# Performance work log

Hardware: AMD Instinct MI355X
Metric: run time of the kernel (lower is better)

## Reference

```python
import jax, jax.numpy as jnp
import numpy as np

M_PER_GROUP = 16
EPS = 0.001


def setup_inputs() -> dict:
    key = jax.random.key(0)
    x = jax.random.normal(key, (32, 64, 64, 256), dtype=jnp.float32)
    return {"x": x}


def reference(x) -> jnp.ndarray:
    # x: [B, W, H, C] (NHWC). Training-phase path, decomposition='cholesky', renorm=False.
    b, w, h, c = x.shape
    groups = c // M_PER_GROUP
    n = b * w * h  # samples per channel

    # [C, B*W*H]
    x_flat = jnp.transpose(x, (3, 0, 1, 2)).reshape(c, -1)
    mean = jnp.mean(x_flat, axis=1, keepdims=True)          # [C, 1]
    f = x_flat - mean                                        # [C, N]

    # per-group covariance: [G, m, N] -> [G, m, m]
    fg = f.reshape(groups, M_PER_GROUP, -1)
    denom = jnp.float32(n) - 1.0
    cov = jnp.einsum('gmn,gkn->gmk', fg, fg) / denom
    eye = jnp.eye(M_PER_GROUP, dtype=x.dtype)
    cov = (1.0 - EPS) * cov + EPS * eye
    # NOTE: the original TF code divides by (N-1) a second time after shrinkage;
    # reproduced faithfully here.
    cov = cov / denom

    # batched Cholesky + triangular solve: inv_sqrt = L^{-1}
    chol = jnp.linalg.cholesky(cov)                          # [G, m, m], lower
    inv_sqrt = jax.vmap(
        lambda L: jax.scipy.linalg.solve_triangular(L, eye, lower=True)
    )(chol)                                                  # [G, m, m]

    # whiten: [G, m, m] @ [G, m, N] -> [G, m, N]
    f_hat = jnp.einsum('gmk,gkn->gmn', inv_sqrt, fg)
    out = f_hat.reshape(c, b, w, h)
    return jnp.transpose(out, (1, 2, 3, 0))
```

## Files before the change

### kernel.cpp

```cpp
#include <hip/hip_runtime.h>


#define NROWS   131072
#define DENOMF  131071.0f
#define EPSV    0.001f

#define OFF_INV    0
#define OFF_BIAS   4096
#define OFF_RED    4352
#define OFF_PART   151808
#define GS2        9216

typedef __attribute__((ext_vector_type(8))) short bf16x8;
typedef __attribute__((ext_vector_type(4))) float f32x4;
typedef __attribute__((ext_vector_type(4))) unsigned int u32x4;

__device__ __forceinline__ unsigned int fbits(float v) {
    return __builtin_bit_cast(unsigned int, v);
}
__device__ __forceinline__ float bfloat(unsigned int u) {
    return __builtin_bit_cast(float, u);
}

__device__ __forceinline__ void gload_lds16(float* lds, const float* g) {
    __builtin_amdgcn_global_load_lds(
        (const __attribute__((address_space(1))) unsigned int*)g,
        (__attribute__((address_space(3))) unsigned int*)lds, 16, 0, 0);
}

struct Row8 { float a, b, c, d, e, f, g, h; };

__device__ __forceinline__ void cvt8(const Row8 r, bf16x8& hv, bf16x8& lv, float& s) {
    s += ((r.a + r.b) + (r.c + r.d)) + ((r.e + r.f) + (r.g + r.h));
    const unsigned int ua = fbits(r.a), ub = fbits(r.b), uc = fbits(r.c), ud = fbits(r.d);
    const unsigned int ue = fbits(r.e), uf = fbits(r.f), ug = fbits(r.g), uh = fbits(r.h);
    u32x4 hp;
    hp.x = (ub & 0xFFFF0000u) | (ua >> 16);
    hp.y = (ud & 0xFFFF0000u) | (uc >> 16);
    hp.z = (uf & 0xFFFF0000u) | (ue >> 16);
    hp.w = (uh & 0xFFFF0000u) | (ug >> 16);
    const float da = r.a - bfloat(ua & 0xFFFF0000u);
    const float db = r.b - bfloat(ub & 0xFFFF0000u);
    const float dc = r.c - bfloat(uc & 0xFFFF0000u);
    const float dd = r.d - bfloat(ud & 0xFFFF0000u);
    const float de = r.e - bfloat(ue & 0xFFFF0000u);
    const float df = r.f - bfloat(uf & 0xFFFF0000u);
    const float dg = r.g - bfloat(ug & 0xFFFF0000u);
    const float dh = r.h - bfloat(uh & 0xFFFF0000u);
    u32x4 lp;
    lp.x = (fbits(db) & 0xFFFF0000u) | (fbits(da) >> 16);
    lp.y = (fbits(dd) & 0xFFFF0000u) | (fbits(dc) >> 16);
    lp.z = (fbits(df) & 0xFFFF0000u) | (fbits(de) >> 16);
    lp.w = (fbits(dh) & 0xFFFF0000u) | (fbits(dg) >> 16);
    hv = __builtin_bit_cast(bf16x8, hp);
    lv = __builtin_bit_cast(bf16x8, lp);
}

__global__ __launch_bounds__(512, 2) void k1_stats(const float* __restrict__ x,
                                                   float* __restrict__ ws, int NB) {
    __shared__ float xt[2][64 * 260];
    const int tid = threadIdx.x;
    const int lane = tid & 63, wv = tid >> 6;
    const int slot = lane >> 4;
    const int TPB = (NROWS / 64) / NB;
    const size_t tile0 = (size_t)blockIdx.x * TPB;

    const int g0 = wv * 2;
    const int rb0 = g0 * 16 + (lane & 15);
    const int roA0 = (slot * 8 + ((0 + 2 * slot) & 7)) * 260 + rb0;
    const int roA1 = (slot * 8 + ((1 + 2 * slot) & 7)) * 260 + rb0;
    const int roA2 = (slot * 8 + ((2 + 2 * slot) & 7)) * 260 + rb0;
    const int roA3 = (slot * 8 + ((3 + 2 * slot) & 7)) * 260 + rb0;
    const int roA4 = (slot * 8 + ((4 + 2 * slot) & 7)) * 260 + rb0;
    const int roA5 = (slot * 8 + ((5 + 2 * slot) & 7)) * 260 + rb0;
    const int roA6 = (slot * 8 + ((6 + 2 * slot) & 7)) * 260 + rb0;
    const int roA7 = (slot * 8 + ((7 + 2 * slot) & 7)) * 260 + rb0;
    const int roB0 = roA0 + 32 * 260, roB1 = roA1 + 32 * 260;
    const int roB2 = roA2 + 32 * 260, roB3 = roA3 + 32 * 260;
    const int roB4 = roA4 + 32 * 260, roB5 = roA5 + 32 * 260;
    const int roB6 = roA6 + 32 * 260, roB7 = roA7 + 32 * 260;

    f32x4 hh0 = {0,0,0,0}, hl0 = {0,0,0,0}, ll0 = {0,0,0,0};
    f32x4 hh1 = {0,0,0,0}, hl1 = {0,0,0,0}, ll1 = {0,0,0,0};
    float s0 = 0.f, s1 = 0.f;

#define STAGE(B, T)                                                           \
    {                                                                         \
        const float* gp = x + ((tile0 + (T)) * 64 + (size_t)(wv * 8)) * 256   \
                            + (size_t)lane * 4;                               \
        float* lb = &xt[B][(wv * 8) * 260];                                   \
        gload_lds16(lb + 0 * 260, gp + 0 * 256);                              \
        gload_lds16(lb + 1 * 260, gp + 1 * 256);                              \
        gload_lds16(lb + 2 * 260, gp + 2 * 256);                              \
        gload_lds16(lb + 3 * 260, gp + 3 * 256);                              \
        gload_lds16(lb + 4 * 260, gp + 4 * 256);                              \
        gload_lds16(lb + 5 * 260, gp + 5 * 256);                              \
        gload_lds16(lb + 6 * 260, gp + 6 * 256);                              \
        gload_lds16(lb + 7 * 260, gp + 7 * 256);                              \
    }
#define PROCG(BUF, U, G, AHH, AHL, ALL, S)                                    \
    {                                                                         \
        const float* bp = &xt[BUF][0];                                        \
        Row8 r;                                                               \
        r.a = bp[ro##U##0 + (G) * 16]; r.b = bp[ro##U##1 + (G) * 16];         \
        r.c = bp[ro##U##2 + (G) * 16]; r.d = bp[ro##U##3 + (G) * 16];         \
        r.e = bp[ro##U##4 + (G) * 16]; r.f = bp[ro##U##5 + (G) * 16];         \
        r.g = bp[ro##U##6 + (G) * 16]; r.h = bp[ro##U##7 + (G) * 16];         \
        bf16x8 hv, lv;                                                        \
        cvt8(r, hv, lv, S);                                                   \
        AHH = __builtin_amdgcn_mfma_f32_16x16x32_bf16(hv, hv, AHH, 0, 0, 0);  \
        AHL = __builtin_amdgcn_mfma_f32_16x16x32_bf16(hv, lv, AHL, 0, 0, 0);  \
        ALL = __builtin_amdgcn_mfma_f32_16x16x32_bf16(lv, lv, ALL, 0, 0, 0);  \
    }
#define PROC4(BUF)                                                            \
    PROCG(BUF, A, 0, hh0, hl0, ll0, s0);                                      \
    PROCG(BUF, B, 0, hh0, hl0, ll0, s0);                                      \
    PROCG(BUF, A, 1, hh1, hl1, ll1, s1);                                      \
    PROCG(BUF, B, 1, hh1, hl1, ll1, s1);

    STAGE(0, 0);
    for (int t = 0; t < TPB - 1; ++t) {
        __syncthreads();
        STAGE((t + 1) & 1, t + 1);
        PROC4(t & 1);
    }
    __syncthreads();
    PROC4((TPB - 1) & 1);
#undef PROC4
#undef PROCG
#undef STAGE

    float* pb = ws + OFF_PART + (size_t)blockIdx.x * GS2 + (size_t)g0 * 576;
#define STG(G, AHH, AHL, ALL, S)                                              \
    {                                                                         \
        float* pw = pb + (G) * 576;                                           \
        pw[0 * 64 + lane] = AHH[0] + ALL[0];                                  \
        pw[1 * 64 + lane] = AHH[1] + ALL[1];                                  \
        pw[2 * 64 + lane] = AHH[2] + ALL[2];                                  \
        pw[3 * 64 + lane] = AHH[3] + ALL[3];                                  \
        pw[4 * 64 + lane] = AHL[0]; pw[5 * 64 + lane] = AHL[1];               \
        pw[6 * 64 + lane] = AHL[2]; pw[7 * 64 + lane] = AHL[3];               \
        pw[8 * 64 + lane] = S;                                                \
    }
    STG(0, hh0, hl0, ll0, s0);
    STG(1, hh1, hl1, ll1, s1);
#undef STG
}

__global__ __launch_bounds__(256, 4) void k2_reduce(float* __restrict__ ws, int NB) {
    const int t = blockIdx.x * 256 + threadIdx.x;
    if (t >= GS2) return;
    const int per = NB / 16;
    const float* p = ws + OFF_PART + (size_t)(blockIdx.y * per) * GS2 + t;
    float sum = 0.f;
#pragma unroll 8
    for (int b = 0; b < per; ++b) sum += p[(size_t)b * GS2];
    ws[OFF_RED + (size_t)blockIdx.y * GS2 + t] = sum;
}

__device__ __forceinline__ void chol_from_sg(const float* sg, int g, int tid,
                                             float* __restrict__ ws) {
    const int ii = tid & 15;
    const float inv_denom = 1.0f / DENOMF;
    const float cs_ii = sg[512 + ii] + sg[512 + 16 + ii] +
                        sg[512 + 32 + ii] + sg[512 + 48 + ii];
    const float mu_l = cs_ii * (1.0f / (float)NROWS);

#define GIDX2(T, I, J) ((T) * 256 + ((I) & 3) * 64 + ((((I) >> 2)) << 4) + (J))
    float arow[16];
#pragma unroll
    for (int kk = 0; kk < 16; ++kk) {
        float G = sg[GIDX2(0, ii, kk)] + sg[GIDX2(1, ii, kk)] + sg[GIDX2(1, kk, ii)];
        float mu_k = __shfl(mu_l, kk, 64);
        float cv = (G - (float)NROWS * mu_l * mu_k) * inv_denom;
        cv = cv * (1.0f - EPSV) + ((kk == ii) ? EPSV : 0.0f);
        arow[kk] = cv * inv_denom;
    }
#undef GIDX2

    float lrow[16];
#pragma unroll
    for (int j = 0; j < 16; ++j) {
        float diag = __shfl(arow[j], j, 64);
        float ljj  = sqrtf(diag);
        float lij  = (ii == j) ? ljj : arow[j] / ljj;
        lrow[j] = lij;
#pragma unroll
        for (int k = j + 1; k < 16; ++k) {
            float lkj = __shfl(lij, k, 64);
            arow[k] = fmaf(-lij, lkj, arow[k]);
        }
    }

    float xcol[16];
#pragma unroll
    for (int i2 = 0; i2 < 16; ++i2) {
        float ssum = (ii == i2) ? 1.0f : 0.0f;
#pragma unroll
        for (int k = 0; k < 16; ++k) {
            if (k < i2) {
                float Lik = __shfl(lrow[k], i2, 64);
                ssum = fmaf(-Lik, xcol[k], ssum);
            }
        }
        float Lii = __shfl(lrow[i2], i2, 64);
        xcol[i2] = (i2 >= ii) ? ssum / Lii : 0.0f;
    }

    float* invg = ws + OFF_INV + g * 256;
#pragma unroll
    for (int i2 = 0; i2 < 16; ++i2) {
        if (tid < 16) invg[i2 * 16 + tid] = xcol[i2];
        float bi = xcol[i2] * mu_l;
        bi += __shfl_xor(bi, 1, 64);
        bi += __shfl_xor(bi, 2, 64);
        bi += __shfl_xor(bi, 4, 64);
        bi += __shfl_xor(bi, 8, 64);
        if (tid == 0) ws[OFF_BIAS + g * 16 + i2] = bi;
    }
}

__global__ void k2_chol(float* __restrict__ ws, int NB) {
    __shared__ float sg[576];
    const int g = blockIdx.x, tid = threadIdx.x;

    for (int e = tid; e < 576; e += 64) {
        float v = 0.f;
#pragma unroll
        for (int y = 0; y < 16; ++y)
            v += ws[OFF_RED + (size_t)y * GS2 + g * 576 + e];
        sg[e] = v;
    }
    __syncthreads();
    chol_from_sg(sg, g, tid, ws);
}

template <int CTRL>
__device__ __forceinline__ float dpp1(float v) {
    int iv = __builtin_bit_cast(int, v);
    int r = __builtin_amdgcn_update_dpp(iv, iv, CTRL, 0xF, 0xF, false);
    return __builtin_bit_cast(float, r);
}
template <int CTRL>
__device__ __forceinline__ float4 dpp4(float4 v) {
    float4 r;
    r.x = dpp1<CTRL>(v.x);
    r.y = dpp1<CTRL>(v.y);
    r.z = dpp1<CTRL>(v.z);
    r.w = dpp1<CTRL>(v.w);
    return r;
}

#define DOT4(O, A, V) \
    O = fmaf(A.x, V.x, O); O = fmaf(A.y, V.y, O); \
    O = fmaf(A.z, V.z, O); O = fmaf(A.w, V.w, O)

__global__ __launch_bounds__(256, 4) void k3_apply(const float* __restrict__ x,
                                                   const float* __restrict__ ws,
                                                   float* __restrict__ out) {
    const int tid = threadIdx.x, lane = tid & 63, wv = tid >> 6;
    const int q = lane & 3, g = lane >> 2;

    const float* invg = ws + OFF_INV + g * 256;
#define LOADIR(R, M) \
    *reinterpret_cast<const float4*>(invg + (4 * q + (R)) * 16 + 4 * (q ^ (M)))
    float4 ir00 = LOADIR(0, 0), ir01 = LOADIR(0, 1), ir02 = LOADIR(0, 2), ir03 = LOADIR(0, 3);
    float4 ir10 = LOADIR(1, 0), ir11 = LOADIR(1, 1), ir12 = LOADIR(1, 2), ir13 = LOADIR(1, 3);
    float4 ir20 = LOADIR(2, 0), ir21 = LOADIR(2, 1), ir22 = LOADIR(2, 2), ir23 = LOADIR(2, 3);
    float4 ir30 = LOADIR(3, 0), ir31 = LOADIR(3, 1), ir32 = LOADIR(3, 2), ir33 = LOADIR(3, 3);
#undef LOADIR
    float4 b4 = *reinterpret_cast<const float4*>(ws + OFF_BIAS + g * 16 + 4 * q);

    const int rpb   = NROWS / gridDim.x;
    const int iters = rpb / 4;
    const size_t rowbase = (size_t)blockIdx.x * rpb;
    const float4* xp = reinterpret_cast<const float4*>(x) + rowbase * 64 + lane;
    float4*       op = reinterpret_cast<float4*>(out)     + rowbase * 64 + lane;

    float4 cur = xp[(size_t)wv * 64];
    for (int i = 0; i < iters; ++i) {
        const int ip = (i + 1 < iters) ? (i + 1) : (iters - 1);
        float4 nxt = xp[(size_t)(ip * 4 + wv) * 64];

        float4 v0 = cur;
        float4 v1 = dpp4<0xB1>(cur);
        float4 v2 = dpp4<0x4E>(cur);
        float4 v3 = dpp4<0x1B>(cur);

        float o0 = -b4.x, o1 = -b4.y, o2 = -b4.z, o3 = -b4.w;
        DOT4(o0, ir00, v0); DOT4(o0, ir01, v1); DOT4(o0, ir02, v2); DOT4(o0, ir03, v3);
        DOT4(o1, ir10, v0); DOT4(o1, ir11, v1); DOT4(o1, ir12, v2); DOT4(o1, ir13, v3);
        DOT4(o2, ir20, v0); DOT4(o2, ir21, v1); DOT4(o2, ir22, v2); DOT4(o2, ir23, v3);
        DOT4(o3, ir30, v0); DOT4(o3, ir31, v1); DOT4(o3, ir32, v2); DOT4(o3, ir33, v3);

        op[(size_t)(i * 4 + wv) * 64] = make_float4(o0, o1, o2, o3);
        cur = nxt;
    }
}

extern "C" void kernel_launch(void* const* d_in, const int* in_sizes, int n_in,
                              void* d_out, int out_size, void* d_ws, size_t ws_size,
                              hipStream_t stream) {
    const float* x = (const float*)d_in[0];
    float* out = (float*)d_out;
    float* ws  = (float*)d_ws;

    int NB = 128;
    if (ws_size >= (size_t)(OFF_PART + 256 * GS2) * sizeof(float)) NB = 256;

    k1_stats<<<NB, 512, 0, stream>>>(x, ws, NB);
    dim3 rg((GS2 + 255) / 256, 16);
    k2_reduce<<<rg, 256, 0, stream>>>(ws, NB);
    k2_chol<<<16, 64, 0, stream>>>(ws, NB);
    k3_apply<<<1024, 256, 0, stream>>>(x, ws, out);
}
```

Measured before the change: 89.80 us.

## Use 32x32x16 MFMA over group pairs for covariance Gram accumulation

```diff
diff --git a/kernel.cpp b/kernel.cpp
--- a/kernel.cpp
+++ b/kernel.cpp
@@ -8,12 +8,13 @@
 #define OFF_INV    0
 #define OFF_BIAS   4096
 #define OFF_RED    4352
-#define OFF_PART   151808
-#define GS2        9216
-
-typedef __attribute__((ext_vector_type(8))) short bf16x8;
-typedef __attribute__((ext_vector_type(4))) float f32x4;
-typedef __attribute__((ext_vector_type(4))) unsigned int u32x4;
+#define OFF_PART   274688
+#define GS3        16896
+#define PWN3       2112
+
+typedef __attribute__((ext_vector_type(8)))  short bf16x8;
+typedef __attribute__((ext_vector_type(16))) float f32x16;
+typedef __attribute__((ext_vector_type(4)))  unsigned int u32x4;
 
 __device__ __forceinline__ unsigned int fbits(float v) {
     return __builtin_bit_cast(unsigned int, v);
@@ -61,62 +62,46 @@
     __shared__ float xt[2][64 * 260];
     const int tid = threadIdx.x;
     const int lane = tid & 63, wv = tid >> 6;
-    const int slot = lane >> 4;
     const int TPB = (NROWS / 64) / NB;
     const size_t tile0 = (size_t)blockIdx.x * TPB;
 
-    const int g0 = wv * 2;
-    const int rb0 = g0 * 16 + (lane & 15);
-    const int roA0 = (slot * 8 + ((0 + 2 * slot) & 7)) * 260 + rb0;
-    const int roA1 = (slot * 8 + ((1 + 2 * slot) & 7)) * 260 + rb0;
-    const int roA2 = (slot * 8 + ((2 + 2 * slot) & 7)) * 260 + rb0;
-    const int roA3 = (slot * 8 + ((3 + 2 * slot) & 7)) * 260 + rb0;
-    const int roA4 = (slot * 8 + ((4 + 2 * slot) & 7)) * 260 + rb0;
-    const int roA5 = (slot * 8 + ((5 + 2 * slot) & 7)) * 260 + rb0;
-    const int roA6 = (slot * 8 + ((6 + 2 * slot) & 7)) * 260 + rb0;
-    const int roA7 = (slot * 8 + ((7 + 2 * slot) & 7)) * 260 + rb0;
-    const int roB0 = roA0 + 32 * 260, roB1 = roA1 + 32 * 260;
-    const int roB2 = roA2 + 32 * 260, roB3 = roA3 + 32 * 260;
-    const int roB4 = roA4 + 32 * 260, roB5 = roA5 + 32 * 260;
-    const int roB6 = roA6 + 32 * 260, roB7 = roA7 + 32 * 260;
-
-    f32x4 hh0 = {0,0,0,0}, hl0 = {0,0,0,0}, ll0 = {0,0,0,0};
-    f32x4 hh1 = {0,0,0,0}, hl1 = {0,0,0,0}, ll1 = {0,0,0,0};
-    float s0 = 0.f, s1 = 0.f;
+    const int gp = wv;
+    const int hb = (lane >> 5) * 2080 + gp * 32 + (lane & 31);
+
+    f32x16 aHH, aHL, aLL;
+#pragma unroll
+    for (int r = 0; r < 16; ++r) { aHH[r] = 0.f; aHL[r] = 0.f; aLL[r] = 0.f; }
+    float s = 0.f;
 
 #define STAGE(B, T)                                                           \
     {                                                                         \
-        const float* gp = x + ((tile0 + (T)) * 64 + (size_t)(wv * 8)) * 256   \
-                            + (size_t)lane * 4;                               \
+        const float* gpv = x + ((tile0 + (T)) * 64 + (size_t)(wv * 8)) * 256  \
+                             + (size_t)lane * 4;                              \
         float* lb = &xt[B][(wv * 8) * 260];                                   \
-        gload_lds16(lb + 0 * 260, gp + 0 * 256);                              \
-        gload_lds16(lb + 1 * 260, gp + 1 * 256);                              \
-        gload_lds16(lb + 2 * 260, gp + 2 * 256);                              \
-        gload_lds16(lb + 3 * 260, gp + 3 * 256);                              \
-        gload_lds16(lb + 4 * 260, gp + 4 * 256);                              \
-        gload_lds16(lb + 5 * 260, gp + 5 * 256);                              \
-        gload_lds16(lb + 6 * 260, gp + 6 * 256);                              \
-        gload_lds16(lb + 7 * 260, gp + 7 * 256);                              \
-    }
-#define PROCG(BUF, U, G, AHH, AHL, ALL, S)                                    \
+        gload_lds16(lb + 0 * 260, gpv + 0 * 256);                             \
+        gload_lds16(lb + 1 * 260, gpv + 1 * 256);                             \
+        gload_lds16(lb + 2 * 260, gpv + 2 * 256);                             \
+        gload_lds16(lb + 3 * 260, gpv + 3 * 256);                             \
+        gload_lds16(lb + 4 * 260, gpv + 4 * 256);                             \
+        gload_lds16(lb + 5 * 260, gpv + 5 * 256);                             \
+        gload_lds16(lb + 6 * 260, gpv + 6 * 256);                             \
+        gload_lds16(lb + 7 * 260, gpv + 7 * 256);                             \
+    }
+#define PROCU(BUF, U)                                                         \
     {                                                                         \
-        const float* bp = &xt[BUF][0];                                        \
+        const float* bp = &xt[BUF][(U) * 4160] + hb;                          \
         Row8 r;                                                               \
-        r.a = bp[ro##U##0 + (G) * 16]; r.b = bp[ro##U##1 + (G) * 16];         \
-        r.c = bp[ro##U##2 + (G) * 16]; r.d = bp[ro##U##3 + (G) * 16];         \
-        r.e = bp[ro##U##4 + (G) * 16]; r.f = bp[ro##U##5 + (G) * 16];         \
-        r.g = bp[ro##U##6 + (G) * 16]; r.h = bp[ro##U##7 + (G) * 16];         \
+        r.a = bp[0 * 260]; r.b = bp[1 * 260]; r.c = bp[2 * 260];              \
+        r.d = bp[3 * 260]; r.e = bp[4 * 260]; r.f = bp[5 * 260];              \
+        r.g = bp[6 * 260]; r.h = bp[7 * 260];                                 \
         bf16x8 hv, lv;                                                        \
-        cvt8(r, hv, lv, S);                                                   \
-        AHH = __builtin_amdgcn_mfma_f32_16x16x32_bf16(hv, hv, AHH, 0, 0, 0);  \
-        AHL = __builtin_amdgcn_mfma_f32_16x16x32_bf16(hv, lv, AHL, 0, 0, 0);  \
-        ALL = __builtin_amdgcn_mfma_f32_16x16x32_bf16(lv, lv, ALL, 0, 0, 0);  \
+        cvt8(r, hv, lv, s);                                                   \
+        aHH = __builtin_amdgcn_mfma_f32_32x32x16_bf16(hv, hv, aHH, 0, 0, 0);  \
+        aHL = __builtin_amdgcn_mfma_f32_32x32x16_bf16(hv, lv, aHL, 0, 0, 0);  \
+        aLL = __builtin_amdgcn_mfma_f32_32x32x16_bf16(lv, lv, aLL, 0, 0, 0);  \
     }
 #define PROC4(BUF)                                                            \
-    PROCG(BUF, A, 0, hh0, hl0, ll0, s0);                                      \
-    PROCG(BUF, B, 0, hh0, hl0, ll0, s0);                                      \
-    PROCG(BUF, A, 1, hh1, hl1, ll1, s1);                                      \
-    PROCG(BUF, B, 1, hh1, hl1, ll1, s1);
+    PROCU(BUF, 0); PROCU(BUF, 1); PROCU(BUF, 2); PROCU(BUF, 3);
 
     STAGE(0, 0);
     for (int t = 0; t < TPB - 1; ++t) {
@@ -127,56 +112,62 @@
     __syncthreads();
     PROC4((TPB - 1) & 1);
 #undef PROC4
-#undef PROCG
+#undef PROCU
 #undef STAGE
 
-    float* pb = ws + OFF_PART + (size_t)blockIdx.x * GS2 + (size_t)g0 * 576;
-#define STG(G, AHH, AHL, ALL, S)                                              \
-    {                                                                         \
-        float* pw = pb + (G) * 576;                                           \
-        pw[0 * 64 + lane] = AHH[0] + ALL[0];                                  \
-        pw[1 * 64 + lane] = AHH[1] + ALL[1];                                  \
-        pw[2 * 64 + lane] = AHH[2] + ALL[2];                                  \
-        pw[3 * 64 + lane] = AHH[3] + ALL[3];                                  \
-        pw[4 * 64 + lane] = AHL[0]; pw[5 * 64 + lane] = AHL[1];               \
-        pw[6 * 64 + lane] = AHL[2]; pw[7 * 64 + lane] = AHL[3];               \
-        pw[8 * 64 + lane] = S;                                                \
-    }
-    STG(0, hh0, hl0, ll0, s0);
-    STG(1, hh1, hl1, ll1, s1);
-#undef STG
+    float* pw = ws + OFF_PART + (size_t)blockIdx.x * GS3 + (size_t)gp * PWN3;
+#pragma unroll
+    for (int r = 0; r < 16; ++r) {
+        pw[r * 64 + lane]        = aHH[r] + aLL[r];
+        pw[(16 + r) * 64 + lane] = aHL[r];
+    }
+    pw[32 * 64 + lane] = s;
 }
 
 __global__ __launch_bounds__(256, 4) void k2_reduce(float* __restrict__ ws, int NB) {
     const int t = blockIdx.x * 256 + threadIdx.x;
-    if (t >= GS2) return;
+    if (t >= GS3) return;
     const int per = NB / 16;
-    const float* p = ws + OFF_PART + (size_t)(blockIdx.y * per) * GS2 + t;
+    const float* p = ws + OFF_PART + (size_t)(blockIdx.y * per) * GS3 + t;
     float sum = 0.f;
 #pragma unroll 8
-    for (int b = 0; b < per; ++b) sum += p[(size_t)b * GS2];
-    ws[OFF_RED + (size_t)blockIdx.y * GS2 + t] = sum;
-}
-
-__device__ __forceinline__ void chol_from_sg(const float* sg, int g, int tid,
-                                             float* __restrict__ ws) {
+    for (int b = 0; b < per; ++b) sum += p[(size_t)b * GS3];
+    ws[OFF_RED + (size_t)blockIdx.y * GS3 + t] = sum;
+}
+
+__global__ void k2_chol(float* __restrict__ ws, int NB) {
+    __shared__ float sg[PWN3];
+    const int g = blockIdx.x, tid = threadIdx.x;
+    const int gp = g >> 1, h = g & 1;
+
+    for (int e = tid; e < PWN3; e += 64) {
+        float v = 0.f;
+#pragma unroll
+        for (int y = 0; y < 16; ++y)
+            v += ws[OFF_RED + (size_t)y * GS3 + gp * PWN3 + e];
+        sg[e] = v;
+    }
+    __syncthreads();
+
     const int ii = tid & 15;
     const float inv_denom = 1.0f / DENOMF;
-    const float cs_ii = sg[512 + ii] + sg[512 + 16 + ii] +
-                        sg[512 + 32 + ii] + sg[512 + 48 + ii];
+    const int c32 = 16 * h + ii;
+    const float cs_ii = sg[32 * 64 + c32] + sg[32 * 64 + 32 + c32];
     const float mu_l = cs_ii * (1.0f / (float)NROWS);
 
-#define GIDX2(T, I, J) ((T) * 256 + ((I) & 3) * 64 + ((((I) >> 2)) << 4) + (J))
+#define GIDX3(T, I, J) \
+    (((T) * 16 + ((I) & 3) + 4 * ((I) >> 3)) * 64 + 32 * (((I) >> 2) & 1) + (J))
     float arow[16];
 #pragma unroll
     for (int kk = 0; kk < 16; ++kk) {
-        float G = sg[GIDX2(0, ii, kk)] + sg[GIDX2(1, ii, kk)] + sg[GIDX2(1, kk, ii)];
+        const int I = 16 * h + ii, J = 16 * h + kk;
+        float G = sg[GIDX3(0, I, J)] + sg[GIDX3(1, I, J)] + sg[GIDX3(1, J, I)];
         float mu_k = __shfl(mu_l, kk, 64);
         float cv = (G - (float)NROWS * mu_l * mu_k) * inv_denom;
         cv = cv * (1.0f - EPSV) + ((kk == ii) ? EPSV : 0.0f);
         arow[kk] = cv * inv_denom;
     }
-#undef GIDX2
+#undef GIDX3
 
     float lrow[16];
 #pragma unroll
@@ -218,21 +209,6 @@
         bi += __shfl_xor(bi, 8, 64);
         if (tid == 0) ws[OFF_BIAS + g * 16 + i2] = bi;
     }
-}
-
-__global__ void k2_chol(float* __restrict__ ws, int NB) {
-    __shared__ float sg[576];
-    const int g = blockIdx.x, tid = threadIdx.x;
-
-    for (int e = tid; e < 576; e += 64) {
-        float v = 0.f;
-#pragma unroll
-        for (int y = 0; y < 16; ++y)
-            v += ws[OFF_RED + (size_t)y * GS2 + g * 576 + e];
-        sg[e] = v;
-    }
-    __syncthreads();
-    chol_from_sg(sg, g, tid, ws);
 }
 
 template <int CTRL>
@@ -306,10 +282,10 @@
     float* ws  = (float*)d_ws;
 
     int NB = 128;
-    if (ws_size >= (size_t)(OFF_PART + 256 * GS2) * sizeof(float)) NB = 256;
+    if (ws_size >= (size_t)(OFF_PART + 256 * GS3) * sizeof(float)) NB = 256;
 
     k1_stats<<<NB, 512, 0, stream>>>(x, ws, NB);
-    dim3 rg((GS2 + 255) / 256, 16);
+    dim3 rg((GS3 + 255) / 256, 16);
     k2_reduce<<<rg, 256, 0, stream>>>(ws, NB);
     k2_chol<<<16, 64, 0, stream>>>(ws, NB);
     k3_apply<<<1024, 256, 0, stream>>>(x, ws, out);
```

After: 92.32 us. 1.03x slower.
